# Kernel optimization log

Measured on AMD Instinct MI355X. Metric: run time of the kernel, lower is better.

Reference implementation:

```python
import jax, jax.numpy as jnp
import numpy as np
import math

B, L, D = 4, 2048, 512
H = 8
HD = D // H
K1 = 64  # local_window_size
K2 = 64  # global_window_size


def semi_local_mask(seq_len):
    # Faithful to create_semi_local_mask: anti-diagonal band + global prefix, ANDed with causal tril.
    i = jnp.arange(seq_len)[:, None]
    j = jnp.arange(seq_len)[None, :]
    band = (i + j >= seq_len - K1) & (i + j <= seq_len)
    glob = (j <= K2) & (j <= seq_len - i)
    causal = j <= i
    return (band | glob) & causal  # [L, L] bool


def setup_inputs() -> dict:
    key = jax.random.key(0)
    ks = jax.random.split(key, 8)
    def xavier(k, shape):
        fan_in, fan_out = shape[1], shape[0]
        lim = math.sqrt(6.0 / (fan_in + fan_out))
        return jax.random.uniform(k, shape, jnp.float32, -lim, lim)
    x = jax.random.normal(ks[0], (B, L, D), jnp.float32)
    w_qkv = xavier(ks[1], (3 * D, D)); b_qkv = jnp.zeros((3 * D,), jnp.float32)
    w_u = xavier(ks[2], (D, D));       b_u = jnp.zeros((D,), jnp.float32)
    w_out = xavier(ks[3], (D, D));     b_out = jnp.zeros((D,), jnp.float32)
    return {"x": x, "w_qkv": w_qkv, "b_qkv": b_qkv, "w_u": w_u, "b_u": b_u,
            "w_out": w_out, "b_out": b_out}


def reference(x, w_qkv, b_qkv, w_u, b_u, w_out, b_out):
    Bsz, Lq, Dm = x.shape
    qkv = (x @ w_qkv.T + b_qkv).reshape(Bsz, Lq, 3, H, HD)
    q, k, v = jnp.moveaxis(qkv, 2, 0)            # each [B, L, H, HD]
    q = jnp.transpose(q, (0, 2, 1, 3))           # [B, H, L, HD]
    k = jnp.transpose(k, (0, 2, 1, 3))
    v = jnp.transpose(v, (0, 2, 1, 3))
    u = x @ w_u.T + b_u                          # [B, L, D] (gate values)
    scale = 1.0 / math.sqrt(HD)
    scores = jnp.einsum('bhqd,bhkd->bhqk', q * scale, k)
    mask = semi_local_mask(Lq)                   # [L, L]
    scores = jnp.where(mask[None, None], scores, -jnp.inf)
    attn = jax.nn.softmax(scores, axis=-1)
    out = jnp.einsum('bhqk,bhkd->bhqd', attn, v)
    out = jnp.transpose(out, (0, 2, 1, 3)).reshape(Bsz, Lq, Dm)
    out = jax.nn.silu(out) * u
    return out @ w_out.T + b_out
```

## Files before the change

### kernel.cpp

```cpp
#include <hip/hip_runtime.h>
#include <hip/hip_bf16.h>

typedef __bf16 bf16x8 __attribute__((ext_vector_type(8)));
typedef float f32x4 __attribute__((ext_vector_type(4)));

#define B_ 4
#define L_ 2048
#define D_ 512
#define H_ 8

__device__ __forceinline__ void gl16(const __bf16* g, __bf16* l) {
  __builtin_amdgcn_global_load_lds(
      (const __attribute__((address_space(1))) void*)g,
      (__attribute__((address_space(3))) void*)l, 16, 0, 0);
}

__global__ __launch_bounds__(256) void cvt_pack(
    const float* __restrict__ x, const float* __restrict__ wq,
    const float* __restrict__ wu, const float* __restrict__ wo,
    const float* __restrict__ bq, const float* __restrict__ bu,
    __bf16* __restrict__ xb, __bf16* __restrict__ wcat,
    __bf16* __restrict__ wob, float* __restrict__ bcat)
{
  const int idx8 = blockIdx.x * 256 + threadIdx.x;
  const float* src; __bf16* dst; size_t so, dof;
  if (idx8 < 524288)      { src = x;  dst = xb;   so = (size_t)idx8 * 8;            dof = so; }
  else if (idx8 < 622592) { src = wq; dst = wcat; so = (size_t)(idx8 - 524288) * 8; dof = so; }
  else if (idx8 < 655360) { src = wu; dst = wcat; so = (size_t)(idx8 - 622592) * 8; dof = so + 786432; }
  else                    { src = wo; dst = wob;  so = (size_t)(idx8 - 655360) * 8; dof = so; }
  const float4 lo = *(const float4*)(src + so);
  const float4 hi = *(const float4*)(src + so + 4);
  bf16x8 r;
  r[0] = (__bf16)lo.x; r[1] = (__bf16)lo.y; r[2] = (__bf16)lo.z; r[3] = (__bf16)lo.w;
  r[4] = (__bf16)hi.x; r[5] = (__bf16)hi.y; r[6] = (__bf16)hi.z; r[7] = (__bf16)hi.w;
  *(bf16x8*)(dst + dof) = r;
  if (blockIdx.x == 0) {
#pragma unroll
    for (int e = 0; e < 8; ++e) {
      const int col = threadIdx.x * 8 + e;
      bcat[col] = (col < 1536) ? bq[col] : bu[col - 1536];
    }
  }
}

template <typename TOUT>
__global__ __launch_bounds__(256) void gemm_async(
    const __bf16* __restrict__ A, const __bf16* __restrict__ W,
    const float* __restrict__ bias, TOUT* __restrict__ C,
    int M, int N, int K)
{
  __shared__ __bf16 lA[4096];
  __shared__ __bf16 lB[4096];
  const int t = threadIdx.x;
  const int lane = t & 63;
  const int wave = t >> 6;
  const int bm0 = blockIdx.x * 128;
  const int bn0 = blockIdx.y * 128;
  const int wm = (wave >> 1) * 64;
  const int wn = (wave & 1) * 64;

  f32x4 acc[4][4] = {};

  const __bf16* Ap0 = A + (size_t)(bm0 + (t >> 2)) * K + (t & 3) * 8;
  const __bf16* Bp0 = W + (size_t)(bn0 + (t >> 2)) * K + (t & 3) * 8;
  const size_t r64 = (size_t)64 * K;

  for (int k0 = 0; k0 < K; k0 += 32) {
    __syncthreads();
    gl16(Ap0 + k0,       lA + t * 8);
    gl16(Ap0 + r64 + k0, lA + (t + 256) * 8);
    gl16(Bp0 + k0,       lB + t * 8);
    gl16(Bp0 + r64 + k0, lB + (t + 256) * 8);
    __syncthreads();

    const int r = lane & 15, q = lane >> 4;
    bf16x8 af[4], bfr[4];
#pragma unroll
    for (int mi = 0; mi < 4; ++mi) af[mi] = ((const bf16x8*)lA)[(wm + mi * 16 + r) * 4 + q];
#pragma unroll
    for (int ni = 0; ni < 4; ++ni) bfr[ni] = ((const bf16x8*)lB)[(wn + ni * 16 + r) * 4 + q];
#pragma unroll
    for (int mi = 0; mi < 4; ++mi)
#pragma unroll
      for (int ni = 0; ni < 4; ++ni)
        acc[mi][ni] = __builtin_amdgcn_mfma_f32_16x16x32_bf16(af[mi], bfr[ni], acc[mi][ni], 0, 0, 0);
  }

  const int cc = lane & 15, cq = lane >> 4;
#pragma unroll
  for (int mi = 0; mi < 4; ++mi) {
#pragma unroll
    for (int ni = 0; ni < 4; ++ni) {
      const int gcol = bn0 + wn + ni * 16 + cc;
      const float bv = bias[gcol];
#pragma unroll
      for (int rr = 0; rr < 4; ++rr) {
        const int grow = bm0 + wm + mi * 16 + cq * 4 + rr;
        C[(size_t)grow * N + gcol] = (TOUT)(acc[mi][ni][rr] + bv);
      }
    }
  }
}

#define SP 72
#define QS 2048
__global__ __launch_bounds__(256) void attn_tile(
    const __bf16* __restrict__ qu,
    __bf16* __restrict__ g)
{
  const int qt = blockIdx.x, h = blockIdx.y, b = blockIdx.z;
  const int t = threadIdx.x;
  const int lane = t & 63;
  const int w = t >> 6;
  const int q0 = qt * 64, qmax = q0 + 63;
  const size_t bL = (size_t)b * L_;

  __shared__ __bf16 lK[4096];
  __shared__ __bf16 lV[64 * SP];
  __shared__ __bf16 Pb[64 * SP];

  const int cq = lane >> 4, cc = lane & 15;

  bf16x8 aq0, aq1;
  {
    const __bf16* qsrc = qu + (bL + q0 + w * 16 + cc) * QS + h * 64 + cq * 8;
    aq0 = *(const bf16x8*)qsrc;
    aq1 = *(const bf16x8*)(qsrc + 32);
  }

  float mreg[4], lreg[4];
#pragma unroll
  for (int rr = 0; rr < 4; ++rr) { mreg[rr] = -1e30f; lreg[rr] = 0.f; }
  f32x4 acc_o[4] = {};

  int clist[5]; int ncl = 0;
  clist[ncl++] = 0;
  if (qmax >= 64) clist[ncl++] = 64;
  {
    int lo = 1921 - q0; if (lo < 0) lo = 0; lo &= ~63;
    const int hik = min(qmax, 2048 - q0);
    for (int c = lo; c <= hik; c += 64)
      if (c >= 128) clist[ncl++] = c;
  }

  for (int ci = 0; ci < ncl; ++ci) {
    const int c0 = clist[ci];
    __syncthreads();
    {
      const int row = t >> 2, gb = t & 3;
      const __bf16* src = qu + (bL + c0 + row) * QS + 512 + h * 64;
      bf16x8 k0 = *(const bf16x8*)(src + gb * 8);
      bf16x8 k1 = *(const bf16x8*)(src + gb * 8 + 32);
      char* lkb = (char*)lK;
      const int sw = (row & 7) << 4;
      *(bf16x8*)(lkb + ((row * 128 + gb * 16) ^ sw))      = k0;
      *(bf16x8*)(lkb + ((row * 128 + gb * 16 + 64) ^ sw)) = k1;
    }
    {
      const int key = lane;
      const __bf16* src = qu + (bL + c0 + key) * QS + 1024 + h * 64 + w * 16;
      bf16x8 va = *(const bf16x8*)src;
      bf16x8 vb = *(const bf16x8*)(src + 8);
#pragma unroll
      for (int e = 0; e < 8; ++e) {
        lV[(w * 16 + e) * SP + key]     = va[e];
        lV[(w * 16 + 8 + e) * SP + key] = vb[e];
      }
    }
    __syncthreads();

    f32x4 s[4];
    {
      const char* lkb = (const char*)lK;
#pragma unroll
      for (int nt = 0; nt < 4; ++nt) {
        const int krow = nt * 16 + cc;
        const int sw = (krow & 7) << 4;
        bf16x8 bk0 = *(const bf16x8*)(lkb + ((krow * 128 + cq * 16) ^ sw));
        bf16x8 bk1 = *(const bf16x8*)(lkb + ((krow * 128 + 64 + cq * 16) ^ sw));
        f32x4 a = {};
        a = __builtin_amdgcn_mfma_f32_16x16x32_bf16(aq0, bk0, a, 0, 0, 0);
        a = __builtin_amdgcn_mfma_f32_16x16x32_bf16(aq1, bk1, a, 0, 0, 0);
        s[nt] = a;
      }
    }

#pragma unroll
    for (int nt = 0; nt < 4; ++nt) {
#pragma unroll
      for (int rr = 0; rr < 4; ++rr) {
        const int i = q0 + w * 16 + cq * 4 + rr;
        const int j = c0 + nt * 16 + cc;
        const int ij = i + j;
        const bool valid = (j <= i) &&
            ((ij >= 1984 && ij <= 2048) || (j <= 64 && ij <= 2048));
        s[nt][rr] = valid ? s[nt][rr] * 0.125f : -1e30f;
      }
    }

    f32x4 pm;
#pragma unroll
    for (int rr = 0; rr < 4; ++rr)
      pm[rr] = fmaxf(fmaxf(s[0][rr], s[1][rr]), fmaxf(s[2][rr], s[3][rr]));
#pragma unroll
    for (int m = 1; m < 16; m <<= 1) {
#pragma unroll
      for (int rr = 0; rr < 4; ++rr)
        pm[rr] = fmaxf(pm[rr], __shfl_xor(pm[rr], m, 64));
    }
    float corr[4];
#pragma unroll
    for (int rr = 0; rr < 4; ++rr) {
      const float nm = fmaxf(mreg[rr], pm[rr]);
      corr[rr] = __expf(mreg[rr] - nm);
      mreg[rr] = nm;
    }

    f32x4 ps = {};
#pragma unroll
    for (int nt = 0; nt < 4; ++nt) {
#pragma unroll
      for (int rr = 0; rr < 4; ++rr) {
        const float p = __expf(s[nt][rr] - mreg[rr]);
        ps[rr] += p;
        Pb[(w * 16 + cq * 4 + rr) * SP + nt * 16 + cc] = (__bf16)p;
      }
    }
#pragma unroll
    for (int m = 1; m < 16; m <<= 1) {
#pragma unroll
      for (int rr = 0; rr < 4; ++rr)
        ps[rr] += __shfl_xor(ps[rr], m, 64);
    }
#pragma unroll
    for (int rr = 0; rr < 4; ++rr) lreg[rr] = lreg[rr] * corr[rr] + ps[rr];

    {
      bf16x8 pa0 = *(const bf16x8*)(Pb + (w * 16 + cc) * SP + cq * 8);
      bf16x8 pa1 = *(const bf16x8*)(Pb + (w * 16 + cc) * SP + 32 + cq * 8);
#pragma unroll
      for (int dt = 0; dt < 4; ++dt) {
#pragma unroll
        for (int rr = 0; rr < 4; ++rr) acc_o[dt][rr] *= corr[rr];
        bf16x8 vb0 = *(const bf16x8*)(lV + (dt * 16 + cc) * SP + cq * 8);
        bf16x8 vb1 = *(const bf16x8*)(lV + (dt * 16 + cc) * SP + 32 + cq * 8);
        acc_o[dt] = __builtin_amdgcn_mfma_f32_16x16x32_bf16(pa0, vb0, acc_o[dt], 0, 0, 0);
        acc_o[dt] = __builtin_amdgcn_mfma_f32_16x16x32_bf16(pa1, vb1, acc_o[dt], 0, 0, 0);
      }
    }
  }

#pragma unroll
  for (int dt = 0; dt < 4; ++dt) {
#pragma unroll
    for (int rr = 0; rr < 4; ++rr) {
      const int row16 = cq * 4 + rr;
      const size_t qrow = bL + q0 + w * 16 + row16;
      const int d = dt * 16 + cc;
      const float o = acc_o[dt][rr] / fmaxf(lreg[rr], 1e-30f);
      const float uv = (float)qu[qrow * QS + 1536 + h * 64 + d];
      g[qrow * D_ + h * 64 + d] = (__bf16)(o / (1.f + __expf(-o)) * uv);
    }
  }
}

extern "C" void kernel_launch(void* const* d_in, const int* in_sizes, int n_in,
                              void* d_out, int out_size, void* d_ws, size_t ws_size,
                              hipStream_t stream) {
  const float* x     = (const float*)d_in[0];
  const float* w_qkv = (const float*)d_in[1];
  const float* b_qkv = (const float*)d_in[2];
  const float* w_u   = (const float*)d_in[3];
  const float* b_u   = (const float*)d_in[4];
  const float* w_out = (const float*)d_in[5];
  const float* b_out = (const float*)d_in[6];
  float* out = (float*)d_out;

  char* ws = (char*)d_ws;
  __bf16* xb   = (__bf16*)ws;
  __bf16* wcat = (__bf16*)(ws + 8388608);
  __bf16* wob  = (__bf16*)(ws + 10485760);
  float*  bcat = (float*) (ws + 11010048);
  __bf16* qu   = (__bf16*)(ws + 11018240);
  __bf16* gb   = (__bf16*)(ws + 44572672);

  cvt_pack<<<dim3(2688), dim3(256), 0, stream>>>(
      x, w_qkv, w_u, w_out, b_qkv, b_u, xb, wcat, wob, bcat);
  gemm_async<__bf16><<<dim3(64, 16), dim3(256), 0, stream>>>(
      xb, wcat, bcat, qu, 8192, 2048, 512);
  attn_tile<<<dim3(L_ / 64, H_, B_), dim3(256), 0, stream>>>(qu, gb);
  gemm_async<float><<<dim3(64, 4), dim3(256), 0, stream>>>(
      gb, wob, b_out, out, 8192, 512, 512);
}
```

Measured before the change: 158.2 us.

## Add 256x256-tile double-buffered MFMA GEMM for QKV/gate projection

```diff
diff --git a/kernel.cpp b/kernel.cpp
--- a/kernel.cpp
+++ b/kernel.cpp
@@ -43,6 +43,132 @@
   }
 }
 
+__global__ __launch_bounds__(512, 2) void gemm256(
+    const __bf16* __restrict__ A, const __bf16* __restrict__ W,
+    const float* __restrict__ bias, __bf16* __restrict__ C,
+    int M, int N, int K)
+{
+  extern __shared__ char smem[];
+  const int t = threadIdx.x;
+  const int lane = t & 63;
+  const int wave = t >> 6;
+  const int wm = (wave >> 2) * 128;
+  const int wn = (wave & 3) * 64;
+  const int bm0 = blockIdx.x * 256;
+  const int bn0 = blockIdx.y * 256;
+  const int r = lane & 15, q = lane >> 4;
+  const int nt = K >> 6;
+
+  auto stage = [&](int kt, int p) {
+#pragma unroll
+    for (int j = 0; j < 4; ++j) {
+      const int c = t + j * 512;
+      const int row = c >> 3;
+      const int cs = (c & 7) ^ (row & 7);
+      gl16(A + (size_t)(bm0 + row) * K + kt * 64 + cs * 8,
+           (__bf16*)(smem + p * 32768) + c * 8);
+    }
+#pragma unroll
+    for (int j = 0; j < 4; ++j) {
+      const int c = t + j * 512;
+      const int row = c >> 3;
+      const int cs = (c & 7) ^ (row & 7);
+      gl16(W + (size_t)(bn0 + row) * K + kt * 64 + cs * 8,
+           (__bf16*)(smem + 65536 + p * 32768) + c * 8);
+    }
+  };
+  auto rdA = [&](int p, int mi, int ks) -> bf16x8 {
+    const int row = wm + mi * 16 + r;
+    const int byte = row * 128 + ((ks * 64 + q * 16) ^ ((row & 7) << 4));
+    return *(const bf16x8*)(smem + p * 32768 + byte);
+  };
+  auto rdB = [&](int p, int ni, int ks) -> bf16x8 {
+    const int row = wn + ni * 16 + r;
+    const int byte = row * 128 + ((ks * 64 + q * 16) ^ ((row & 7) << 4));
+    return *(const bf16x8*)(smem + 65536 + p * 32768 + byte);
+  };
+
+  f32x4 acc[8][4] = {};
+
+  stage(0, 0);
+  stage(1, 1);
+
+  for (int kt = 0; kt < nt; ++kt) {
+    const int p = kt & 1;
+    if (kt < nt - 1) asm volatile("s_waitcnt vmcnt(8)" ::: "memory");
+    else             asm volatile("s_waitcnt vmcnt(0)" ::: "memory");
+    __builtin_amdgcn_sched_barrier(0);
+    __builtin_amdgcn_s_barrier();
+    __builtin_amdgcn_sched_barrier(0);
+
+    bf16x8 a03[4][2], a47[4][2], b01[2][2], b23[2][2];
+#pragma unroll
+    for (int mi = 0; mi < 4; ++mi) { a03[mi][0] = rdA(p, mi, 0); a03[mi][1] = rdA(p, mi, 1); }
+#pragma unroll
+    for (int ni = 0; ni < 2; ++ni) { b01[ni][0] = rdB(p, ni, 0); b01[ni][1] = rdB(p, ni, 1); }
+    __builtin_amdgcn_s_setprio(1);
+#pragma unroll
+    for (int mi = 0; mi < 4; ++mi)
+#pragma unroll
+      for (int ni = 0; ni < 2; ++ni) {
+        acc[mi][ni] = __builtin_amdgcn_mfma_f32_16x16x32_bf16(a03[mi][0], b01[ni][0], acc[mi][ni], 0, 0, 0);
+        acc[mi][ni] = __builtin_amdgcn_mfma_f32_16x16x32_bf16(a03[mi][1], b01[ni][1], acc[mi][ni], 0, 0, 0);
+      }
+    __builtin_amdgcn_s_setprio(0);
+#pragma unroll
+    for (int ni = 0; ni < 2; ++ni) { b23[ni][0] = rdB(p, ni + 2, 0); b23[ni][1] = rdB(p, ni + 2, 1); }
+    __builtin_amdgcn_s_setprio(1);
+#pragma unroll
+    for (int mi = 0; mi < 4; ++mi)
+#pragma unroll
+      for (int ni = 0; ni < 2; ++ni) {
+        acc[mi][ni + 2] = __builtin_amdgcn_mfma_f32_16x16x32_bf16(a03[mi][0], b23[ni][0], acc[mi][ni + 2], 0, 0, 0);
+        acc[mi][ni + 2] = __builtin_amdgcn_mfma_f32_16x16x32_bf16(a03[mi][1], b23[ni][1], acc[mi][ni + 2], 0, 0, 0);
+      }
+    __builtin_amdgcn_s_setprio(0);
+#pragma unroll
+    for (int mi = 0; mi < 4; ++mi) { a47[mi][0] = rdA(p, mi + 4, 0); a47[mi][1] = rdA(p, mi + 4, 1); }
+    __builtin_amdgcn_s_setprio(1);
+#pragma unroll
+    for (int mi = 0; mi < 4; ++mi)
+#pragma unroll
+      for (int ni = 0; ni < 2; ++ni) {
+        acc[mi + 4][ni] = __builtin_amdgcn_mfma_f32_16x16x32_bf16(a47[mi][0], b01[ni][0], acc[mi + 4][ni], 0, 0, 0);
+        acc[mi + 4][ni] = __builtin_amdgcn_mfma_f32_16x16x32_bf16(a47[mi][1], b01[ni][1], acc[mi + 4][ni], 0, 0, 0);
+      }
+    __builtin_amdgcn_s_setprio(0);
+    asm volatile("s_waitcnt lgkmcnt(0)" ::: "memory");
+    __builtin_amdgcn_sched_barrier(0);
+    __builtin_amdgcn_s_barrier();
+    __builtin_amdgcn_sched_barrier(0);
+    if (kt + 2 < nt) stage(kt + 2, p);
+    __builtin_amdgcn_s_setprio(1);
+#pragma unroll
+    for (int mi = 0; mi < 4; ++mi)
+#pragma unroll
+      for (int ni = 0; ni < 2; ++ni) {
+        acc[mi + 4][ni + 2] = __builtin_amdgcn_mfma_f32_16x16x32_bf16(a47[mi][0], b23[ni][0], acc[mi + 4][ni + 2], 0, 0, 0);
+        acc[mi + 4][ni + 2] = __builtin_amdgcn_mfma_f32_16x16x32_bf16(a47[mi][1], b23[ni][1], acc[mi + 4][ni + 2], 0, 0, 0);
+      }
+    __builtin_amdgcn_s_setprio(0);
+  }
+
+  const int cc = lane & 15, cq = lane >> 4;
+#pragma unroll
+  for (int mi = 0; mi < 8; ++mi) {
+#pragma unroll
+    for (int ni = 0; ni < 4; ++ni) {
+      const int gcol = bn0 + wn + ni * 16 + cc;
+      const float bv = bias[gcol];
+#pragma unroll
+      for (int rr = 0; rr < 4; ++rr) {
+        const int grow = bm0 + wm + mi * 16 + cq * 4 + rr;
+        C[(size_t)grow * N + gcol] = (__bf16)(acc[mi][ni][rr] + bv);
+      }
+    }
+  }
+}
+
 template <typename TOUT>
 __global__ __launch_bounds__(256) void gemm_async(
     const __bf16* __restrict__ A, const __bf16* __restrict__ W,
@@ -284,9 +410,16 @@
   __bf16* qu   = (__bf16*)(ws + 11018240);
   __bf16* gb   = (__bf16*)(ws + 44572672);
 
+  static bool attr_done = []() {
+    hipFuncSetAttribute((const void*)gemm256,
+                        hipFuncAttributeMaxDynamicSharedMemorySize, 131072);
+    return true;
+  }();
+  (void)attr_done;
+
   cvt_pack<<<dim3(2688), dim3(256), 0, stream>>>(
       x, w_qkv, w_u, w_out, b_qkv, b_u, xb, wcat, wob, bcat);
-  gemm_async<__bf16><<<dim3(64, 16), dim3(256), 0, stream>>>(
+  gemm256<<<dim3(32, 8), dim3(512), 131072, stream>>>(
       xb, wcat, bcat, qu, 8192, 2048, 512);
   attn_tile<<<dim3(L_ / 64, H_, B_), dim3(256), 0, stream>>>(qu, gb);
   gemm_async<float><<<dim3(64, 4), dim3(256), 0, stream>>>(
```

After: 148.5 us. 6.1% less time.
